# Kernel optimization log

Hardware: AMD Instinct MI355X
Metric: run time of the kernel (lower is better)

## Reference

```python
import jax, jax.numpy as jnp
import numpy as np

N_NODES = 50000
N_EDGES = 800000
D = 128
N_RELS = 460  # 2 * num_rels
N_BASES = 32
SUBMAT = D // N_BASES  # 4
INV_TEMP = 0.1


def setup_inputs() -> dict:
    key = jax.random.key(0)
    ks = jax.random.split(key, 16)
    return {
        "h": jax.random.normal(ks[0], (N_NODES, D), jnp.float32),
        "first_prev": jax.random.normal(ks[1], (N_NODES, D), jnp.float32),
        "second_prev": jax.random.normal(ks[2], (N_NODES, D), jnp.float32),
        "time_diff": jax.random.uniform(ks[3], (N_NODES, 1), jnp.float32),
        "edge_src": jax.random.randint(ks[4], (N_EDGES,), 0, N_NODES, jnp.int32),
        "edge_dst": jax.random.randint(ks[5], (N_EDGES,), 0, N_NODES, jnp.int32),
        "edge_type": jax.random.randint(ks[6], (N_EDGES,), 0, N_RELS, jnp.int32),
        "edge_norm": jax.random.uniform(ks[7], (N_EDGES, 1), jnp.float32),
        "node_norm": jax.random.uniform(ks[8], (N_NODES, 1), jnp.float32),
        "W1": jax.random.normal(ks[9], (N_RELS, N_BASES * SUBMAT * SUBMAT), jnp.float32) * 0.05,
        "W2": jax.random.normal(ks[10], (N_RELS, N_BASES * SUBMAT * SUBMAT), jnp.float32) * 0.05,
        "loop_w1": jax.random.normal(ks[11], (D, D), jnp.float32) * 0.05,
        "loop_w2": jax.random.normal(ks[12], (D, D), jnp.float32) * 0.05,
        "time_w1": jax.random.normal(ks[13], (D, D), jnp.float32) * 0.05,
        "time_w2": jax.random.normal(ks[14], (D, D), jnp.float32) * 0.05,
    }


def _drgcn_layer(h, prev, time_diff, W, loop_w, time_w,
                 edge_src, edge_dst, edge_type, edge_norm, node_norm, activate):
    n = h.shape[0]
    # self-loop message (dropout is identity in eval)
    loop_msg = h @ loop_w                                     # [N, D]
    # block-diagonal per-edge message: gather relation blocks + batched small matmul
    w = W[edge_type].reshape(-1, N_BASES, SUBMAT, SUBMAT)     # [E, B, si, so]
    hs = h[edge_src].reshape(-1, N_BASES, SUBMAT)             # [E, B, si]
    msg = jnp.einsum('ebi,ebio->ebo', hs, w).reshape(-1, h.shape[1])  # [E, D]
    msg = msg * edge_norm                                     # per-edge norm
    agg = jax.ops.segment_sum(msg, edge_dst, num_segments=n)  # scatter-sum to dst
    agg = agg * node_norm                                     # apply_func node norm
    # time-decay residual + self-loop (bias=None in this config)
    out = agg + (prev @ time_w) * jnp.exp(-time_diff * INV_TEMP) + loop_msg
    if activate:
        out = jax.nn.relu(out)
    return out


def reference(h, first_prev, second_prev, time_diff,
              edge_src, edge_dst, edge_type, edge_norm, node_norm,
              W1, W2, loop_w1, loop_w2, time_w1, time_w2):
    h1 = _drgcn_layer(h, first_prev, time_diff, W1, loop_w1, time_w1,
                      edge_src, edge_dst, edge_type, edge_norm, node_norm, activate=False)
    h2 = _drgcn_layer(h1, second_prev, time_diff, W2, loop_w2, time_w2,
                      edge_src, edge_dst, edge_type, edge_norm, node_norm, activate=True)
    return (h1, h2)
```

## Files before the change

### kernel.cpp

```cpp
#include <hip/hip_runtime.h>

#define NN 50000
#define NE 800000
#define DD 128
#define NPAD 50176
#define NBLK_SCAN 196

typedef __attribute__((ext_vector_type(8))) short short8;
typedef __attribute__((ext_vector_type(4))) float f32x4;

static __device__ __forceinline__ float b2f(unsigned short u) {
    return __builtin_bit_cast(float, (unsigned)u << 16);
}
static __device__ __forceinline__ float b2f_lo(unsigned u) {
    return __builtin_bit_cast(float, u << 16);
}
static __device__ __forceinline__ float b2f_hi(unsigned u) {
    return __builtin_bit_cast(float, u & 0xffff0000u);
}
static __device__ __forceinline__ unsigned short f2b(float f) {
    unsigned u = __builtin_bit_cast(unsigned, f);
    u += 0x7FFFu + ((u >> 16) & 1u);
    return (unsigned short)(u >> 16);
}

__global__ __launch_bounds__(256) void k_hist(
    const int* __restrict__ edst, int* __restrict__ cnt)
{
    const int e = blockIdx.x * 256 + threadIdx.x;
    atomicAdd(&cnt[edst[e]], 1);
}

__global__ __launch_bounds__(256) void k_scan_a(
    const int* __restrict__ cnt, int* __restrict__ bsum)
{
    __shared__ int s[256];
    const int t = threadIdx.x;
    s[t] = cnt[blockIdx.x * 256 + t];
    __syncthreads();
    for (int d = 128; d > 0; d >>= 1) {
        if (t < d) s[t] += s[t + d];
        __syncthreads();
    }
    if (t == 0) bsum[blockIdx.x] = s[0];
}

__global__ __launch_bounds__(256) void k_scan_b(int* __restrict__ bsum)
{
    __shared__ int s[256];
    const int t = threadIdx.x;
    s[t] = (t < NBLK_SCAN) ? bsum[t] : 0;
    __syncthreads();
    for (int d = 1; d < 256; d <<= 1) {
        int v = (t >= d) ? s[t - d] : 0;
        __syncthreads();
        s[t] += v;
        __syncthreads();
    }
    bsum[t] = (t == 0) ? 0 : s[t - 1];
}

__global__ __launch_bounds__(256) void k_scan_c(
    const int* __restrict__ cnt, const int* __restrict__ bsum,
    int* __restrict__ off, int* __restrict__ cur)
{
    __shared__ int s[256];
    const int t = threadIdx.x;
    const int i = blockIdx.x * 256 + t;
    const int c = cnt[i];
    s[t] = c;
    __syncthreads();
    for (int d = 1; d < 256; d <<= 1) {
        int v = (t >= d) ? s[t - d] : 0;
        __syncthreads();
        s[t] += v;
        __syncthreads();
    }
    const int ex = bsum[blockIdx.x] + s[t] - c;
    off[i] = ex;
    cur[i] = ex;
}

__global__ __launch_bounds__(256) void k_scatter(
    const int* __restrict__ esrc, const int* __restrict__ edst,
    const int* __restrict__ etyp, const float* __restrict__ enorm,
    int* __restrict__ cur, int4* __restrict__ sedge)
{
    const int e = blockIdx.x * 256 + threadIdx.x;
    const int pos = atomicAdd(&cur[edst[e]], 1);
    sedge[pos] = make_int4(esrc[e], etyp[e],
                           __builtin_bit_cast(int, enorm[e]), 0);
}

__global__ __launch_bounds__(256) void conv_x(
    const float* __restrict__ x, const float* __restrict__ fprev,
    const float* __restrict__ sprev, const float* __restrict__ tdiff,
    unsigned short* __restrict__ X1, unsigned short* __restrict__ X2)
{
    const int idx = blockIdx.x * 256 + threadIdx.x;
    const int n = idx >> 7, j = idx & 127;
    const float d = __expf(-tdiff[n] * 0.1f);
    X1[(size_t)n * 256 + j]       = f2b(x[(size_t)n * 128 + j]);
    X1[(size_t)n * 256 + 128 + j] = f2b(fprev[(size_t)n * 128 + j] * d);
    X2[(size_t)n * 256 + 128 + j] = f2b(sprev[(size_t)n * 128 + j] * d);
}

__global__ __launch_bounds__(256) void conv_w2(
    const float* __restrict__ W1, const float* __restrict__ W2,
    unsigned short* __restrict__ W1b, unsigned short* __restrict__ W2b)
{
    const int i = blockIdx.x * 256 + threadIdx.x;
    if (i < 460 * 512) W1b[i] = f2b(W1[i]);
    else               W2b[i - 460 * 512] = f2b(W2[i - 460 * 512]);
}

__global__ __launch_bounds__(256) void pack_wc2(
    const float* __restrict__ lw1, const float* __restrict__ tw1,
    const float* __restrict__ lw2, const float* __restrict__ tw2,
    unsigned short* __restrict__ Wp1, unsigned short* __restrict__ Wp2)
{
    const int g = blockIdx.x * 256 + threadIdx.x;
    const int c = g & 4095;
    const float* lw = (g < 4096) ? lw1 : lw2;
    const float* tw = (g < 4096) ? tw1 : tw2;
    unsigned short* Wp = (g < 4096) ? Wp1 : Wp2;
    const int ct = c >> 9, ks = (c >> 6) & 7, lane = c & 63;
    const int col = ct * 16 + (lane & 15);
    unsigned short* o = Wp + (size_t)c * 8;
    #pragma unroll
    for (int i = 0; i < 8; ++i) {
        const int k = ks * 32 + (lane >> 4) * 8 + i;
        const float v = (k < 128) ? lw[(size_t)k * 128 + col]
                                  : tw[(size_t)(k - 128) * 128 + col];
        o[i] = f2b(v);
    }
}

__device__ __forceinline__ void agg_edge(
    const unsigned short* __restrict__ x,
    const unsigned short* __restrict__ Wb,
    const int4* __restrict__ sedge, int i,
    int woff, int l, float4& acc)
{
    const int4 e = sedge[i];
    const int src = __builtin_amdgcn_readfirstlane(e.x);
    const int typ = __builtin_amdgcn_readfirstlane(e.y);
    const float nr = __builtin_bit_cast(float, __builtin_amdgcn_readfirstlane(e.z));
    const unsigned hw = ((const unsigned*)(x + (size_t)src * 256))[l];
    const uint4 wv = *(const uint4*)(Wb + (size_t)typ * 512 + woff);
    const float h0 = b2f_lo(hw) * nr;
    const float h1 = b2f_hi(hw) * nr;
    acc.x += h0 * b2f_lo(wv.x) + h1 * b2f_lo(wv.z);
    acc.y += h0 * b2f_hi(wv.x) + h1 * b2f_hi(wv.z);
    acc.z += h0 * b2f_lo(wv.y) + h1 * b2f_lo(wv.w);
    acc.w += h0 * b2f_hi(wv.y) + h1 * b2f_hi(wv.w);
}

__global__ __launch_bounds__(256) void k_agg2(
    const unsigned short* __restrict__ x,
    const int4*  __restrict__ sedge,
    const int*   __restrict__ off,
    const unsigned short* __restrict__ Wb,
    const float* __restrict__ nnorm,
    float*       __restrict__ agg)
{
    const int l = threadIdx.x & 63;
    const int n = blockIdx.x * 4 + (threadIdx.x >> 6);
    const int beg = off[n], end = off[n + 1];
    const int woff = (l >> 1) * 16 + (l & 1) * 8;

    float4 a0 = {0,0,0,0}, a1 = {0,0,0,0}, a2 = {0,0,0,0}, a3 = {0,0,0,0};

    int i = beg;
    for (; i + 4 <= end; i += 4) {
        agg_edge(x, Wb, sedge, i,     woff, l, a0);
        agg_edge(x, Wb, sedge, i + 1, woff, l, a1);
        agg_edge(x, Wb, sedge, i + 2, woff, l, a2);
        agg_edge(x, Wb, sedge, i + 3, woff, l, a3);
    }
    for (; i < end; ++i) agg_edge(x, Wb, sedge, i, woff, l, a0);

    float4 s;
    s.x = (a0.x + a1.x) + (a2.x + a3.x);
    s.y = (a0.y + a1.y) + (a2.y + a3.y);
    s.z = (a0.z + a1.z) + (a2.z + a3.z);
    s.w = (a0.w + a1.w) + (a2.w + a3.w);
    s.x += __shfl_xor(s.x, 1);
    s.y += __shfl_xor(s.y, 1);
    s.z += __shfl_xor(s.z, 1);
    s.w += __shfl_xor(s.w, 1);

    const float nn = nnorm[n];
    const float e0 = (l & 1) ? s.z : s.x;
    const float e1 = (l & 1) ? s.w : s.y;
    float2* outp = (float2*)(agg + (size_t)n * DD + (l >> 1) * 4 + (l & 1) * 2);
    *outp = make_float2(e0 * nn, e1 * nn);
}

template<int ACT, int WRITE_NEXT>
__global__ __launch_bounds__(256) void combine_mfma(
    const float* __restrict__ agg,
    const unsigned short* __restrict__ X,
    const unsigned short* __restrict__ Wp,
    float* __restrict__ out,
    unsigned short* __restrict__ Xnext)
{
    const int t = threadIdx.x;
    const int l = t & 63;
    const int w = t >> 6;
    const int wr = w >> 1, wc = w & 1;
    const int l15 = l & 15, lhi = l >> 4;
    const int rowbase = blockIdx.x * 64 + wr * 32;

    f32x4 acc[2][4] = {};

    const int ar0 = min(rowbase + l15, NN - 1);
    const int ar1 = min(rowbase + 16 + l15, NN - 1);
    const unsigned short* a0p = X + (size_t)ar0 * 256 + lhi * 8;
    const unsigned short* a1p = X + (size_t)ar1 * 256 + lhi * 8;
    const unsigned short* bp  = Wp + (size_t)(wc * 4) * 8 * 512 + (size_t)l * 8;

    #pragma unroll
    for (int ks = 0; ks < 8; ++ks) {
        const short8 a0 = *(const short8*)(a0p + ks * 32);
        const short8 a1 = *(const short8*)(a1p + ks * 32);
        #pragma unroll
        for (int ct = 0; ct < 4; ++ct) {
            const short8 b = *(const short8*)(bp + (size_t)(ct * 8 + ks) * 512);
            acc[0][ct] = __builtin_amdgcn_mfma_f32_16x16x32_bf16(a0, b, acc[0][ct], 0, 0, 0);
            acc[1][ct] = __builtin_amdgcn_mfma_f32_16x16x32_bf16(a1, b, acc[1][ct], 0, 0, 0);
        }
    }

    #pragma unroll
    for (int rg = 0; rg < 2; ++rg) {
        #pragma unroll
        for (int q = 0; q < 4; ++q) {
            const int row = rowbase + rg * 16 + lhi * 4 + q;
            if (row < NN) {
                #pragma unroll
                for (int ct = 0; ct < 4; ++ct) {
                    const int col = wc * 64 + ct * 16 + l15;
                    float v = agg[(size_t)row * DD + col] + acc[rg][ct][q];
                    if (ACT) v = fmaxf(v, 0.f);
                    out[(size_t)row * DD + col] = v;
                    if (WRITE_NEXT) Xnext[(size_t)row * 256 + col] = f2b(v);
                }
            }
        }
    }
}

__device__ __forceinline__ float pick4(float4 v, int o) {
    float a = (o & 1) ? v.y : v.x;
    float b = (o & 1) ? v.w : v.z;
    return (o & 2) ? b : a;
}

__global__ __launch_bounds__(256) void k_agg_t2(
    const float* __restrict__ x, const int4* __restrict__ sedge,
    const int* __restrict__ off, const float* __restrict__ W,
    float* __restrict__ agg)
{
    const int lane = threadIdx.x & 63;
    const int n    = blockIdx.x * 4 + (threadIdx.x >> 6);
    const int beg = off[n], end = off[n + 1];
    float4 acca = make_float4(0.f, 0.f, 0.f, 0.f);
    float4 accb = make_float4(0.f, 0.f, 0.f, 0.f);
    for (int i = beg; i < end; ++i) {
        const int4 e = sedge[i];
        const float nr = __builtin_bit_cast(float, e.z);
        const float* wr = W + (size_t)e.y * 512 + 4 * lane;
        const float4 wa = *(const float4*)wr;
        const float4 wb = *(const float4*)(wr + 256);
        const float* hr = x + (size_t)e.x * DD;
        const float ha = hr[lane] * nr;
        const float hb = hr[64 + lane] * nr;
        acca.x += ha * wa.x; acca.y += ha * wa.y; acca.z += ha * wa.z; acca.w += ha * wa.w;
        accb.x += hb * wb.x; accb.y += hb * wb.y; accb.z += hb * wb.z; accb.w += hb * wb.w;
    }
    #pragma unroll
    for (int d = 1; d <= 2; d <<= 1) {
        acca.x += __shfl_xor(acca.x, d); acca.y += __shfl_xor(acca.y, d);
        acca.z += __shfl_xor(acca.z, d); acca.w += __shfl_xor(acca.w, d);
        accb.x += __shfl_xor(accb.x, d); accb.y += __shfl_xor(accb.y, d);
        accb.z += __shfl_xor(accb.z, d); accb.w += __shfl_xor(accb.w, d);
    }
    const int o = lane & 3;
    agg[(size_t)n * DD + lane]      = pick4(acca, o);
    agg[(size_t)n * DD + 64 + lane] = pick4(accb, o);
}

__global__ __launch_bounds__(256) void edge_msg(
    const float* __restrict__ x, const int* __restrict__ esrc,
    const int* __restrict__ edst, const int* __restrict__ etyp,
    const float* __restrict__ enorm, const float* __restrict__ W,
    float* __restrict__ agg)
{
    const int t  = threadIdx.x;
    const int le = t >> 7;
    const int j  = t & 127;
    const int e  = blockIdx.x * 2 + le;
    __shared__ float sh[2][DD];
    sh[le][j] = x[(size_t)esrc[e] * DD + j];
    __syncthreads();
    const int b = j >> 2, o = j & 3;
    const float* wr = W + (size_t)etyp[e] * 512 + b * 16 + o;
    const float4 hv = *(const float4*)&sh[le][b * 4];
    float m = hv.x * wr[0] + hv.y * wr[4] + hv.z * wr[8] + hv.w * wr[12];
    m *= enorm[e];
    atomicAdd(&agg[(size_t)edst[e] * DD + j], m);
}

template<int ACT>
__global__ __launch_bounds__(256) void combine(
    float* __restrict__ out, const float* __restrict__ x,
    const float* __restrict__ prev, const float* __restrict__ tdiff,
    const float* __restrict__ nnorm, const float* __restrict__ lw,
    const float* __restrict__ tw)
{
    const int t = threadIdx.x;
    const int j = t & 127;
    const int r = t >> 7;
    const int base = blockIdx.x * 8;
    __shared__ float sh[8][DD];
    __shared__ float sp[8][DD];
    #pragma unroll
    for (int q = 0; q < 4; ++q) {
        const int m = q * 2 + r;
        const int n = base + m;
        const float decay = __expf(-tdiff[n] * 0.1f);
        sh[m][j] = x[(size_t)n * DD + j];
        sp[m][j] = prev[(size_t)n * DD + j] * decay;
    }
    __syncthreads();
    float acc[4] = {0.f, 0.f, 0.f, 0.f};
    for (int k = 0; k < DD; k += 4) {
        float wl[4], wt[4];
        #pragma unroll
        for (int kk = 0; kk < 4; ++kk) {
            wl[kk] = lw[(size_t)(k + kk) * DD + j];
            wt[kk] = tw[(size_t)(k + kk) * DD + j];
        }
        #pragma unroll
        for (int q = 0; q < 4; ++q) {
            const int m = q * 2 + r;
            const float4 a = *(const float4*)&sh[m][k];
            const float4 p = *(const float4*)&sp[m][k];
            acc[q] += a.x * wl[0] + a.y * wl[1] + a.z * wl[2] + a.w * wl[3]
                    + p.x * wt[0] + p.y * wt[1] + p.z * wt[2] + p.w * wt[3];
        }
    }
    #pragma unroll
    for (int q = 0; q < 4; ++q) {
        const int m = q * 2 + r;
        const int n = base + m;
        float v = out[(size_t)n * DD + j] * nnorm[n] + acc[q];
        if (ACT) v = fmaxf(v, 0.f);
        out[(size_t)n * DD + j] = v;
    }
}

extern "C" void kernel_launch(void* const* d_in, const int* in_sizes, int n_in,
                              void* d_out, int out_size, void* d_ws, size_t ws_size,
                              hipStream_t stream) {
    const float* h     = (const float*)d_in[0];
    const float* fprev = (const float*)d_in[1];
    const float* sprev = (const float*)d_in[2];
    const float* tdiff = (const float*)d_in[3];
    const int*   esrc  = (const int*)d_in[4];
    const int*   edst  = (const int*)d_in[5];
    const int*   etyp  = (const int*)d_in[6];
    const float* enorm = (const float*)d_in[7];
    const float* nnorm = (const float*)d_in[8];
    const float* W1    = (const float*)d_in[9];
    const float* W2    = (const float*)d_in[10];
    const float* lw1   = (const float*)d_in[11];
    const float* lw2   = (const float*)d_in[12];
    const float* tw1   = (const float*)d_in[13];
    const float* tw2   = (const float*)d_in[14];

    float* h1 = (float*)d_out;
    float* h2 = h1 + (size_t)NN * DD;
    const size_t layer_bytes = (size_t)NN * DD * sizeof(float);

    char* wsp = (char*)d_ws;
    int*   cnt   = (int*)wsp;  wsp += (size_t)NPAD * 4;
    int*   off   = (int*)wsp;  wsp += (size_t)NPAD * 4;
    int*   cur   = (int*)wsp;  wsp += (size_t)NPAD * 4;
    int*   bsum  = (int*)wsp;  wsp += 256 * 4;
    int4*  sedge = (int4*)wsp; wsp += (size_t)NE * 16;
    const size_t ws_sorted = (size_t)(wsp - (char*)d_ws);
    unsigned short* X1   = (unsigned short*)wsp; wsp += (size_t)NN * 256 * 2;
    unsigned short* X2   = (unsigned short*)wsp; wsp += (size_t)NN * 256 * 2;
    unsigned short* Wc1p = (unsigned short*)wsp; wsp += 4096 * 8 * 2;
    unsigned short* Wc2p = (unsigned short*)wsp; wsp += 4096 * 8 * 2;
    unsigned short* W1b  = (unsigned short*)wsp; wsp += (size_t)460 * 512 * 2;
    unsigned short* W2b  = (unsigned short*)wsp; wsp += (size_t)460 * 512 * 2;
    const size_t ws_full = (size_t)(wsp - (char*)d_ws);

    const int grid_mm = (NN + 63) / 64;

    if (ws_size >= ws_full) {
        hipMemsetAsync(cnt, 0, (size_t)NPAD * 4, stream);
        k_hist   <<<NE / 256, 256, 0, stream>>>(edst, cnt);
        k_scan_a <<<NBLK_SCAN, 256, 0, stream>>>(cnt, bsum);
        k_scan_b <<<1, 256, 0, stream>>>(bsum);
        k_scan_c <<<NBLK_SCAN, 256, 0, stream>>>(cnt, bsum, off, cur);
        k_scatter<<<NE / 256, 256, 0, stream>>>(esrc, edst, etyp, enorm, cur, sedge);
        conv_x  <<<NN * DD / 256, 256, 0, stream>>>(h, fprev, sprev, tdiff, X1, X2);
        conv_w2 <<<2 * 460 * 512 / 256, 256, 0, stream>>>(W1, W2, W1b, W2b);
        pack_wc2<<<32, 256, 0, stream>>>(lw1, tw1, lw2, tw2, Wc1p, Wc2p);
        k_agg2<<<NN / 4, 256, 0, stream>>>(X1, sedge, off, W1b, nnorm, h1);
        combine_mfma<0, 1><<<grid_mm, 256, 0, stream>>>(h1, X1, Wc1p, h1, X2);
        k_agg2<<<NN / 4, 256, 0, stream>>>(X2, sedge, off, W2b, nnorm, h2);
        combine_mfma<1, 0><<<grid_mm, 256, 0, stream>>>(h2, X2, Wc2p, h2, nullptr);
    } else if (ws_size >= ws_sorted) {
        hipMemsetAsync(cnt, 0, (size_t)NPAD * 4, stream);
        k_hist   <<<NE / 256, 256, 0, stream>>>(edst, cnt);
        k_scan_a <<<NBLK_SCAN, 256, 0, stream>>>(cnt, bsum);
        k_scan_b <<<1, 256, 0, stream>>>(bsum);
        k_scan_c <<<NBLK_SCAN, 256, 0, stream>>>(cnt, bsum, off, cur);
        k_scatter<<<NE / 256, 256, 0, stream>>>(esrc, edst, etyp, enorm, cur, sedge);
        k_agg_t2<<<NN / 4, 256, 0, stream>>>(h, sedge, off, W1, h1);
        combine<0><<<NN / 8, 256, 0, stream>>>(h1, h, fprev, tdiff, nnorm, lw1, tw1);
        k_agg_t2<<<NN / 4, 256, 0, stream>>>(h1, sedge, off, W2, h2);
        combine<1><<<NN / 8, 256, 0, stream>>>(h2, h1, sprev, tdiff, nnorm, lw2, tw2);
    } else {
        hipMemsetAsync(h1, 0, layer_bytes, stream);
        edge_msg<<<NE / 2, 256, 0, stream>>>(h, esrc, edst, etyp, enorm, W1, h1);
        combine<0><<<NN / 8, 256, 0, stream>>>(h1, h, fprev, tdiff, nnorm, lw1, tw1);
        hipMemsetAsync(h2, 0, layer_bytes, stream);
        edge_msg<<<NE / 2, 256, 0, stream>>>(h1, esrc, edst, etyp, enorm, W2, h2);
        combine<1><<<NN / 8, 256, 0, stream>>>(h2, h1, sprev, tdiff, nnorm, lw2, tw2);
    }
}
```

Measured before the change: 429.8 us.

## Switch aggregation to edge-balanced chunks with boundary atomics and fuse weight prep

```diff
diff --git a/kernel.cpp b/kernel.cpp
--- a/kernel.cpp
+++ b/kernel.cpp
@@ -5,6 +5,8 @@
 #define DD 128
 #define NPAD 50176
 #define NBLK_SCAN 196
+#define EPW 64
+#define NCHUNK ((NE + EPW - 1) / EPW)
 
 typedef __attribute__((ext_vector_type(8))) short short8;
 typedef __attribute__((ext_vector_type(4))) float f32x4;
@@ -87,9 +89,10 @@
     int* __restrict__ cur, int4* __restrict__ sedge)
 {
     const int e = blockIdx.x * 256 + threadIdx.x;
-    const int pos = atomicAdd(&cur[edst[e]], 1);
+    const int d = edst[e];
+    const int pos = atomicAdd(&cur[d], 1);
     sedge[pos] = make_int4(esrc[e], etyp[e],
-                           __builtin_bit_cast(int, enorm[e]), 0);
+                           __builtin_bit_cast(int, enorm[e]), d);
 }
 
 __global__ __launch_bounds__(256) void conv_x(
@@ -105,96 +108,105 @@
     X2[(size_t)n * 256 + 128 + j] = f2b(sprev[(size_t)n * 128 + j] * d);
 }
 
-__global__ __launch_bounds__(256) void conv_w2(
+__global__ __launch_bounds__(256) void k_wprep(
     const float* __restrict__ W1, const float* __restrict__ W2,
-    unsigned short* __restrict__ W1b, unsigned short* __restrict__ W2b)
-{
-    const int i = blockIdx.x * 256 + threadIdx.x;
-    if (i < 460 * 512) W1b[i] = f2b(W1[i]);
-    else               W2b[i - 460 * 512] = f2b(W2[i - 460 * 512]);
-}
-
-__global__ __launch_bounds__(256) void pack_wc2(
+    unsigned short* __restrict__ W1b, unsigned short* __restrict__ W2b,
     const float* __restrict__ lw1, const float* __restrict__ tw1,
     const float* __restrict__ lw2, const float* __restrict__ tw2,
     unsigned short* __restrict__ Wp1, unsigned short* __restrict__ Wp2)
 {
-    const int g = blockIdx.x * 256 + threadIdx.x;
-    const int c = g & 4095;
-    const float* lw = (g < 4096) ? lw1 : lw2;
-    const float* tw = (g < 4096) ? tw1 : tw2;
-    unsigned short* Wp = (g < 4096) ? Wp1 : Wp2;
-    const int ct = c >> 9, ks = (c >> 6) & 7, lane = c & 63;
-    const int col = ct * 16 + (lane & 15);
-    unsigned short* o = Wp + (size_t)c * 8;
-    #pragma unroll
-    for (int i = 0; i < 8; ++i) {
-        const int k = ks * 32 + (lane >> 4) * 8 + i;
-        const float v = (k < 128) ? lw[(size_t)k * 128 + col]
-                                  : tw[(size_t)(k - 128) * 128 + col];
-        o[i] = f2b(v);
-    }
-}
-
-__device__ __forceinline__ void agg_edge(
-    const unsigned short* __restrict__ x,
-    const unsigned short* __restrict__ Wb,
-    const int4* __restrict__ sedge, int i,
-    int woff, int l, float4& acc)
-{
-    const int4 e = sedge[i];
-    const int src = __builtin_amdgcn_readfirstlane(e.x);
-    const int typ = __builtin_amdgcn_readfirstlane(e.y);
-    const float nr = __builtin_bit_cast(float, __builtin_amdgcn_readfirstlane(e.z));
-    const unsigned hw = ((const unsigned*)(x + (size_t)src * 256))[l];
-    const uint4 wv = *(const uint4*)(Wb + (size_t)typ * 512 + woff);
-    const float h0 = b2f_lo(hw) * nr;
-    const float h1 = b2f_hi(hw) * nr;
-    acc.x += h0 * b2f_lo(wv.x) + h1 * b2f_lo(wv.z);
-    acc.y += h0 * b2f_hi(wv.x) + h1 * b2f_hi(wv.z);
-    acc.z += h0 * b2f_lo(wv.y) + h1 * b2f_lo(wv.w);
-    acc.w += h0 * b2f_hi(wv.y) + h1 * b2f_hi(wv.w);
-}
-
-__global__ __launch_bounds__(256) void k_agg2(
-    const unsigned short* __restrict__ x,
-    const int4*  __restrict__ sedge,
-    const int*   __restrict__ off,
-    const unsigned short* __restrict__ Wb,
-    const float* __restrict__ nnorm,
-    float*       __restrict__ agg)
-{
-    const int l = threadIdx.x & 63;
-    const int n = blockIdx.x * 4 + (threadIdx.x >> 6);
-    const int beg = off[n], end = off[n + 1];
-    const int woff = (l >> 1) * 16 + (l & 1) * 8;
-
-    float4 a0 = {0,0,0,0}, a1 = {0,0,0,0}, a2 = {0,0,0,0}, a3 = {0,0,0,0};
-
-    int i = beg;
-    for (; i + 4 <= end; i += 4) {
-        agg_edge(x, Wb, sedge, i,     woff, l, a0);
-        agg_edge(x, Wb, sedge, i + 1, woff, l, a1);
-        agg_edge(x, Wb, sedge, i + 2, woff, l, a2);
-        agg_edge(x, Wb, sedge, i + 3, woff, l, a3);
-    }
-    for (; i < end; ++i) agg_edge(x, Wb, sedge, i, woff, l, a0);
-
-    float4 s;
-    s.x = (a0.x + a1.x) + (a2.x + a3.x);
-    s.y = (a0.y + a1.y) + (a2.y + a3.y);
-    s.z = (a0.z + a1.z) + (a2.z + a3.z);
-    s.w = (a0.w + a1.w) + (a2.w + a3.w);
+    const int gb = blockIdx.x;
+    if (gb < 1840) {
+        const int i = gb * 256 + threadIdx.x;
+        if (i < 460 * 512) W1b[i] = f2b(W1[i]);
+        else               W2b[i - 460 * 512] = f2b(W2[i - 460 * 512]);
+    } else {
+        const int g = (gb - 1840) * 256 + threadIdx.x;
+        const int c = g & 4095;
+        const float* lw = (g < 4096) ? lw1 : lw2;
+        const float* tw = (g < 4096) ? tw1 : tw2;
+        unsigned short* Wp = (g < 4096) ? Wp1 : Wp2;
+        const int ct = c >> 9, ks = (c >> 6) & 7, lane = c & 63;
+        const int col = ct * 16 + (lane & 15);
+        unsigned short* o = Wp + (size_t)c * 8;
+        #pragma unroll
+        for (int i = 0; i < 8; ++i) {
+            const int k = ks * 32 + (lane >> 4) * 8 + i;
+            const float v = (k < 128) ? lw[(size_t)k * 128 + col]
+                                      : tw[(size_t)(k - 128) * 128 + col];
+            o[i] = f2b(v);
+        }
+    }
+}
+
+__device__ __forceinline__ void flush_seg(
+    float4 s, int dst, bool part, int l,
+    const float* __restrict__ nnorm, float* __restrict__ agg)
+{
     s.x += __shfl_xor(s.x, 1);
     s.y += __shfl_xor(s.y, 1);
     s.z += __shfl_xor(s.z, 1);
     s.w += __shfl_xor(s.w, 1);
-
-    const float nn = nnorm[n];
-    const float e0 = (l & 1) ? s.z : s.x;
-    const float e1 = (l & 1) ? s.w : s.y;
-    float2* outp = (float2*)(agg + (size_t)n * DD + (l >> 1) * 4 + (l & 1) * 2);
-    *outp = make_float2(e0 * nn, e1 * nn);
+    const float nn = nnorm[dst];
+    const float e0 = ((l & 1) ? s.z : s.x) * nn;
+    const float e1 = ((l & 1) ? s.w : s.y) * nn;
+    float* p = agg + (size_t)dst * DD + (l >> 1) * 4 + (l & 1) * 2;
+    if (part) {
+        atomicAdd(p, e0);
+        atomicAdd(p + 1, e1);
+    } else {
+        *(float2*)p = make_float2(e0, e1);
+    }
+}
+
+__global__ __launch_bounds__(256) void k_agg3(
+    const unsigned short* __restrict__ x,
+    const int4*  __restrict__ sedge,
+    const unsigned short* __restrict__ Wb,
+    const float* __restrict__ nnorm,
+    float*       __restrict__ agg)
+{
+    const int l = threadIdx.x & 63;
+    const int chunk = blockIdx.x * 4 + (threadIdx.x >> 6);
+    const int cbeg = chunk * EPW;
+    if (cbeg >= NE) return;
+    const int cend = min(cbeg + EPW, NE);
+    const int woff = (l >> 1) * 16 + (l & 1) * 8;
+
+    const int prevdst = (cbeg > 0)  ? sedge[cbeg - 1].w : -1;
+    const int nextdst = (cend < NE) ? sedge[cend].w     : -2;
+
+    int4 e = sedge[cbeg];
+    unsigned hw = ((const unsigned*)(x + (size_t)e.x * 256))[l];
+    uint4 wv = *(const uint4*)(Wb + (size_t)e.y * 512 + woff);
+
+    int dcur = e.w;
+    bool part = (dcur == prevdst);
+    float4 acc = make_float4(0.f, 0.f, 0.f, 0.f);
+
+    for (int i = cbeg; i < cend; ++i) {
+        const int j = min(i + 1, cend - 1);
+        const int4 en = sedge[j];
+        const unsigned hwn = ((const unsigned*)(x + (size_t)en.x * 256))[l];
+        const uint4 wvn = *(const uint4*)(Wb + (size_t)en.y * 512 + woff);
+
+        if (e.w != dcur) {
+            flush_seg(acc, dcur, part, l, nnorm, agg);
+            acc = make_float4(0.f, 0.f, 0.f, 0.f);
+            dcur = e.w;
+            part = false;
+        }
+        const float nr = __builtin_bit_cast(float, e.z);
+        const float h0 = b2f_lo(hw) * nr;
+        const float h1 = b2f_hi(hw) * nr;
+        acc.x += h0 * b2f_lo(wv.x) + h1 * b2f_lo(wv.z);
+        acc.y += h0 * b2f_hi(wv.x) + h1 * b2f_hi(wv.z);
+        acc.z += h0 * b2f_lo(wv.y) + h1 * b2f_lo(wv.w);
+        acc.w += h0 * b2f_hi(wv.y) + h1 * b2f_hi(wv.w);
+
+        e = en; hw = hwn; wv = wvn;
+    }
+    flush_seg(acc, dcur, part || (dcur == nextdst), l, nnorm, agg);
 }
 
 template<int ACT, int WRITE_NEXT>
@@ -400,6 +412,7 @@
     const size_t ws_full = (size_t)(wsp - (char*)d_ws);
 
     const int grid_mm = (NN + 63) / 64;
+    const int grid_agg = (NCHUNK + 3) / 4;
 
     if (ws_size >= ws_full) {
         hipMemsetAsync(cnt, 0, (size_t)NPAD * 4, stream);
@@ -408,12 +421,14 @@
         k_scan_b <<<1, 256, 0, stream>>>(bsum);
         k_scan_c <<<NBLK_SCAN, 256, 0, stream>>>(cnt, bsum, off, cur);
         k_scatter<<<NE / 256, 256, 0, stream>>>(esrc, edst, etyp, enorm, cur, sedge);
-        conv_x  <<<NN * DD / 256, 256, 0, stream>>>(h, fprev, sprev, tdiff, X1, X2);
-        conv_w2 <<<2 * 460 * 512 / 256, 256, 0, stream>>>(W1, W2, W1b, W2b);
-        pack_wc2<<<32, 256, 0, stream>>>(lw1, tw1, lw2, tw2, Wc1p, Wc2p);
-        k_agg2<<<NN / 4, 256, 0, stream>>>(X1, sedge, off, W1b, nnorm, h1);
+        conv_x <<<NN * DD / 256, 256, 0, stream>>>(h, fprev, sprev, tdiff, X1, X2);
+        k_wprep<<<1872, 256, 0, stream>>>(W1, W2, W1b, W2b,
+                                          lw1, tw1, lw2, tw2, Wc1p, Wc2p);
+        hipMemsetAsync(h1, 0, layer_bytes, stream);
+        hipMemsetAsync(h2, 0, layer_bytes, stream);
+        k_agg3<<<grid_agg, 256, 0, stream>>>(X1, sedge, W1b, nnorm, h1);
         combine_mfma<0, 1><<<grid_mm, 256, 0, stream>>>(h1, X1, Wc1p, h1, X2);
-        k_agg2<<<NN / 4, 256, 0, stream>>>(X2, sedge, off, W2b, nnorm, h2);
+        k_agg3<<<grid_agg, 256, 0, stream>>>(X2, sedge, W2b, nnorm, h2);
         combine_mfma<1, 0><<<grid_mm, 256, 0, stream>>>(h2, X2, Wc2p, h2, nullptr);
     } else if (ws_size >= ws_sorted) {
         hipMemsetAsync(cnt, 0, (size_t)NPAD * 4, stream);
```

Measured after the change: 487.7 us. +13.5%, slower.
